# Performance work log

Hardware: AMD Instinct MI355X
Metric: run time of the kernel (lower is better)

The kernel has to match this reference:

```python
import jax, jax.numpy as jnp
import numpy as np

N = 20000   # genes
E = 200000  # global edges
P = 300     # pathways
EP = 2000   # edges per pathway (global node indices)
D = 3       # in_dim == number of omics (forced by nn.Linear(3,1))


def setup_inputs():
    key = jax.random.key(0)
    ks = jax.random.split(key, 20)
    f = lambda i, shape: jax.random.normal(ks[i], shape, dtype=jnp.float32) * 0.1
    return {
        "x": f(0, (N, D)),
        "edge_index": jax.random.randint(ks[1], (2, E), 0, N),
        "path_edges": jax.random.randint(ks[2], (P, 2, EP), 0, N),
        "W_pool": f(3, (D, D)), "b_pool": f(4, (D,)),
        "W_self": f(5, (D, D)), "W_neigh": f(6, (D, D)), "b_conv": f(7, (D,)),
        "sub_Wl": f(8, (P, D, D)), "sub_bl": f(9, (P, D)), "sub_Wr": f(10, (P, D, D)),
        "pool_Wrel": f(11, (P, D, 1)), "pool_Wroot": f(12, (P, D, 1)), "pool_b": f(13, (P, 1)),
        "gate_W": f(14, (P, D, 1)), "gate_b": f(15, (P, 1)),
        "lin_W": f(16, (D, 1)), "lin_b": f(17, (1,)),
        "mlp_W": f(18, (P, 1)), "mlp_b": f(19, (1,)),
    }


def reference(x, edge_index, path_edges, W_pool, b_pool, W_self, W_neigh, b_conv,
              sub_Wl, sub_bl, sub_Wr, pool_Wrel, pool_Wroot, pool_b,
              gate_W, gate_b, lin_W, lin_b, mlp_W, mlp_b):
    n = x.shape[0]
    # add_self_loops on the global edge_index
    loops = jnp.arange(n)
    src = jnp.concatenate([edge_index[0], loops])
    dst = jnp.concatenate([edge_index[1], loops])

    # global SAGEConv with 'pool' aggregator: max_j relu(W_pool h_j), then self + neigh
    hp = jax.nn.relu(x @ W_pool + b_pool)                       # [N,D]
    agg = jax.ops.segment_max(hp[src], dst, num_segments=n)     # [N,D] (self-loops -> no empty segments)
    h = jnp.tanh(x @ W_self + agg @ W_neigh + b_conv)           # [N,D]

    k = int(np.ceil(0.8 * n))  # SAGPooling ratio=0.8 over all N nodes (full x is passed per pathway)

    def per_path(pe, Wl, bl, Wr, Wrel, Wroot, pb, gW, gb):
        s, d = pe[0], pe[1]
        # SAGEConv (mean aggr) on pathway subgraph edges over full node set
        msum = jax.ops.segment_sum(h[s], d, num_segments=n)
        cnt = jax.ops.segment_sum(jnp.ones(s.shape, h.dtype), d, num_segments=n)
        mean = msum / jnp.maximum(cnt, 1.0)[:, None]
        xc = jax.nn.relu(mean @ Wl + bl + h @ Wr)               # [N,D]
        # SAGPooling score via GraphConv (add aggr): W_rel * sum_j x_j + W_root * x + b
        asum = jax.ops.segment_sum(xc[s], d, num_segments=n)
        score = (asum @ Wrel + xc @ Wroot + pb)[:, 0]           # [N]
        topv, perm = jax.lax.top_k(score, k)
        xk = xc[perm] * jnp.tanh(topv)[:, None]                 # [k,D]
        # GlobalAttention readout: softmax gate over kept nodes
        gate = jax.nn.softmax((xk @ gW + gb)[:, 0])             # [k]
        return jax.nn.relu(gate @ xk)                            # [D]

    readout = jax.vmap(per_path)(path_edges, sub_Wl, sub_bl, sub_Wr,
                                 pool_Wrel, pool_Wroot, pool_b, gate_W, gate_b)  # [P,D]
    r = jax.nn.relu(readout @ lin_W + lin_b).T                  # [1,P]
    # mlp: Dropout (identity in eval) -> ReLU -> Linear(P,1) -> Sigmoid
    return jax.nn.sigmoid(jax.nn.relu(r) @ mlp_W + mlp_b)       # [1,1]
```

## Files before the change

kernel.cpp:

```cpp
#include <hip/hip_runtime.h>
#include <math.h>

#define MAXM 2048
#define BMW  640
#define BS   1024
#define NB   2048

__device__ __forceinline__ unsigned fkey(float f){
  unsigned u = __float_as_uint(f);
  return (u & 0x80000000u) ? ~u : (u | 0x80000000u);
}
__device__ __forceinline__ int lbin(float sc, float lo, float scl){
  int b = (int)((sc - lo) * scl);
  return b < 0 ? 0 : (b > NB-1 ? NB-1 : b);
}
__device__ __forceinline__ float fast_tanh(float x){
  float e = __expf(2.f*x);
  return 1.f - 2.f*__builtin_amdgcn_rcpf(e + 1.f);
}
__device__ __forceinline__ void hp_eval(const float* __restrict__ x, int i,
                                        const float* __restrict__ Wp,
                                        const float* __restrict__ bp, float* o){
  float x0 = x[i*3+0], x1 = x[i*3+1], x2 = x[i*3+2];
  #pragma unroll
  for (int j = 0; j < 3; ++j)
    o[j] = fmaxf(x0*Wp[0*3+j] + x1*Wp[1*3+j] + x2*Wp[2*3+j] + bp[j], 0.f);
}

__global__ void k_edge(const float* __restrict__ x, const int* __restrict__ ei,
                       const float* __restrict__ Wp, const float* __restrict__ bp,
                       float* __restrict__ agg, float* __restrict__ acc,
                       unsigned* __restrict__ counter, int E){
  if (blockIdx.x == 0 && threadIdx.x == 0){ acc[0] = 0.f; counter[0] = 0u; }
  int e = blockIdx.x*blockDim.x + threadIdx.x;
  if (e >= E) return;
  int s = ei[e], d = ei[E+e];
  float o[3]; hp_eval(x, s, Wp, bp, o);
  #pragma unroll
  for (int j = 0; j < 3; ++j)
    if (o[j] > 0.f && o[j] > agg[d*4+j])
      atomicMax((int*)&agg[d*4+j], __float_as_int(o[j]));
}

__global__ void k_h2(const float* __restrict__ x, float* __restrict__ hb,
                     const float* __restrict__ Wp, const float* __restrict__ bp,
                     const float* __restrict__ Ws, const float* __restrict__ Wn,
                     const float* __restrict__ bc, int N){
  int i = blockIdx.x*blockDim.x + threadIdx.x;
  if (i >= N) return;
  float hp[3]; hp_eval(x, i, Wp, bp, hp);
  float x0 = x[i*3+0], x1 = x[i*3+1], x2 = x[i*3+2];
  float a0 = fmaxf(hb[i*4+0], hp[0]);
  float a1 = fmaxf(hb[i*4+1], hp[1]);
  float a2 = fmaxf(hb[i*4+2], hp[2]);
  float o[3];
  #pragma unroll
  for (int j = 0; j < 3; ++j){
    float v = x0*Ws[0*3+j] + x1*Ws[1*3+j] + x2*Ws[2*3+j]
            + a0*Wn[0*3+j] + a1*Wn[1*3+j] + a2*Wn[2*3+j] + bc[j];
    o[j] = tanhf(v);
  }
  float4 hv; hv.x = o[0]; hv.y = o[1]; hv.z = o[2]; hv.w = 0.f;
  *reinterpret_cast<float4*>(&hb[i*4]) = hv;
}

__global__ void __launch_bounds__(BS)
k_mega(const float* __restrict__ h, const int* __restrict__ pe,
       const float* __restrict__ sWl, const float* __restrict__ sbl, const float* __restrict__ sWr,
       const float* __restrict__ pWrel, const float* __restrict__ pWroot, const float* __restrict__ pB,
       const float* __restrict__ gW, const float* __restrict__ gB,
       const float* __restrict__ linW, const float* __restrict__ linb,
       const float* __restrict__ mlpW, const float* __restrict__ mlpb,
       float* __restrict__ spG, float* __restrict__ acc, unsigned* __restrict__ counter,
       unsigned* __restrict__ out, int N, int EP, int K, int P){
  __shared__ unsigned bm[BMW];
  __shared__ int      wpfx[BMW];
  __shared__ float    msum[MAXM*4];
  __shared__ unsigned scrA[NB];
  __shared__ unsigned scrB[NB];
  __shared__ unsigned candIdx[NB];
  __shared__ float    wredf[(BS/64)*2];
  __shared__ float    wredA[(BS/64)*4];
  __shared__ float    wredB[(BS/64)*4];
  __shared__ float    s_mn, s_mx;
  __shared__ float    s_slo, s_sscl;
  __shared__ float    rlo[3], rsc[3];
  __shared__ int      rb[3];
  __shared__ int      s_r, s_C, s_cc, s_done, s_fused;
  __shared__ unsigned s_uT;

  const int p = blockIdx.x;
  const int tid = threadIdx.x;

  float Wl[9], Wr[9], bl[3], wrel[3], wroot[3], gw[3];
  #pragma unroll
  for (int j = 0; j < 9; ++j){ Wl[j] = sWl[p*9+j]; Wr[j] = sWr[p*9+j]; }
  #pragma unroll
  for (int j = 0; j < 3; ++j){
    bl[j] = sbl[p*3+j]; wrel[j] = pWrel[p*3+j];
    wroot[j] = pWroot[p*3+j]; gw[j] = gW[p*3+j];
  }
  float pbv = pB[p], gbv = gB[p];
  float* sp = spG + (size_t)p*N;

  int*      cnt  = (int*)scrA;
  float*    adot = (float*)scrB;
  unsigned* hist = scrA;
  unsigned* cand = scrB;

  for (int s = tid; s < MAXM; s += BS){
    cnt[s] = 0; adot[s] = 0.f;
    float4 z; z.x = 0.f; z.y = 0.f; z.z = 0.f; z.w = 0.f;
    *reinterpret_cast<float4*>(&msum[s*4]) = z;
  }
  for (int s = tid; s < BMW; s += BS) bm[s] = 0u;
  if (tid == 0){ s_done = 0; s_fused = 0; s_uT = 0u; }
  __syncthreads();

  const int* ps = pe + (size_t)p*2*EP;
  const int* pd = ps + EP;

  for (int e = tid; e < EP; e += BS) atomicOr(&bm[pd[e]>>5], 1u << (pd[e]&31));
  __syncthreads();
  if (tid < 64){
    int l = tid, base = l*10;
    int c[10], s = 0;
    #pragma unroll
    for (int q = 0; q < 10; ++q){ c[q] = __popc(bm[base+q]); s += c[q]; }
    int pre = s;
    #pragma unroll
    for (int off = 1; off < 64; off <<= 1){
      int t = __shfl_up(pre, off);
      if (l >= off) pre += t;
    }
    pre -= s;
    #pragma unroll
    for (int q = 0; q < 10; ++q){ wpfx[base+q] = pre; pre += c[q]; }
  }
  __syncthreads();
  for (int e = tid; e < EP; e += BS){
    int s = ps[e], d = pd[e];
    int r = wpfx[d>>5] + __popc(bm[d>>5] & ((1u << (d&31)) - 1u));
    float4 hs = *reinterpret_cast<const float4*>(&h[s*4]);
    atomicAdd(&cnt[r], 1);
    atomicAdd(&msum[r*4+0], hs.x);
    atomicAdd(&msum[r*4+1], hs.y);
    atomicAdd(&msum[r*4+2], hs.z);
  }
  __syncthreads();
  for (int r = tid; r < MAXM; r += BS){
    int c = cnt[r];
    cnt[r] = 0;
    if (c > 0){
      float inv = 1.f / (float)c;
      msum[r*4+0] *= inv; msum[r*4+1] *= inv; msum[r*4+2] *= inv;
    }
  }
  __syncthreads();
  for (int e = tid; e < EP; e += BS){
    int s = ps[e], d = pd[e];
    float m0=0.f,m1=0.f,m2=0.f;
    unsigned w = bm[s>>5];
    if ((w >> (s&31)) & 1u){
      int rs = wpfx[s>>5] + __popc(w & ((1u << (s&31)) - 1u));
      float4 mv = *reinterpret_cast<const float4*>(&msum[rs*4]);
      m0 = mv.x; m1 = mv.y; m2 = mv.z;
    }
    float4 hv = *reinterpret_cast<const float4*>(&h[s*4]);
    float h0 = hv.x, h1 = hv.y, h2 = hv.z;
    float x0 = fmaxf(m0*Wl[0]+m1*Wl[3]+m2*Wl[6] + bl[0] + h0*Wr[0]+h1*Wr[3]+h2*Wr[6], 0.f);
    float x1 = fmaxf(m0*Wl[1]+m1*Wl[4]+m2*Wl[7] + bl[1] + h0*Wr[1]+h1*Wr[4]+h2*Wr[7], 0.f);
    float x2 = fmaxf(m0*Wl[2]+m1*Wl[5]+m2*Wl[8] + bl[2] + h0*Wr[2]+h1*Wr[5]+h2*Wr[8], 0.f);
    int rd = wpfx[d>>5] + __popc(bm[d>>5] & ((1u << (d&31)) - 1u));
    atomicAdd(&adot[rd], x0*wrel[0] + x1*wrel[1] + x2*wrel[2]);
  }
  __syncthreads();

  {
    int i = (int)(((long long)tid * (long long)N) / BS);
    float m0=0.f,m1=0.f,m2=0.f,ad=0.f;
    unsigned w = bm[i>>5];
    if ((w >> (i&31)) & 1u){
      int r = wpfx[i>>5] + __popc(w & ((1u << (i&31)) - 1u));
      float4 mv = *reinterpret_cast<const float4*>(&msum[r*4]);
      m0 = mv.x; m1 = mv.y; m2 = mv.z;
      ad = adot[r];
    }
    float4 hv = *reinterpret_cast<const float4*>(&h[i*4]);
    float h0 = hv.x, h1 = hv.y, h2 = hv.z;
    float x0 = fmaxf(m0*Wl[0]+m1*Wl[3]+m2*Wl[6] + bl[0] + h0*Wr[0]+h1*Wr[3]+h2*Wr[6], 0.f);
    float x1 = fmaxf(m0*Wl[1]+m1*Wl[4]+m2*Wl[7] + bl[1] + h0*Wr[1]+h1*Wr[4]+h2*Wr[7], 0.f);
    float x2 = fmaxf(m0*Wl[2]+m1*Wl[5]+m2*Wl[8] + bl[2] + h0*Wr[2]+h1*Wr[5]+h2*Wr[8], 0.f);
    float sc = ad + x0*wroot[0]+x1*wroot[1]+x2*wroot[2] + pbv;
    float smn = sc, smx = sc;
    #pragma unroll
    for (int off = 32; off > 0; off >>= 1){
      smn = fminf(smn, __shfl_down(smn, off));
      smx = fmaxf(smx, __shfl_down(smx, off));
    }
    if ((tid & 63) == 0){ int w2 = tid >> 6; wredf[w2*2+0] = smn; wredf[w2*2+1] = smx; }
    __syncthreads();
    if (tid == 0){
      float a = 3.0e38f, b = -3.0e38f;
      for (int w2 = 0; w2 < BS/64; ++w2){
        a = fminf(a, wredf[w2*2+0]); b = fmaxf(b, wredf[w2*2+1]);
      }
      float span = b - a;
      if (!(span > 0.f)) span = fabsf(a)*1e-6f + 1e-30f;
      s_slo = a; s_sscl = 2047.0f / span;
    }
    __syncthreads();
  }
  float lo0, scl0;
  {
    unsigned ulo = __builtin_amdgcn_readfirstlane(__float_as_uint(s_slo));
    unsigned usc = __builtin_amdgcn_readfirstlane(__float_as_uint(s_sscl));
    lo0 = __uint_as_float(ulo); scl0 = __uint_as_float(usc);
  }

  float mn = 3.0e38f, mx = -3.0e38f;
  float tl = 0.f, ta0 = 0.f, ta1 = 0.f, ta2 = 0.f;
  for (int i = tid; i < N; i += BS){
    float m0=0.f,m1=0.f,m2=0.f,ad=0.f;
    unsigned w = bm[i>>5];
    if ((w >> (i&31)) & 1u){
      int r = wpfx[i>>5] + __popc(w & ((1u << (i&31)) - 1u));
      float4 mv = *reinterpret_cast<const float4*>(&msum[r*4]);
      m0 = mv.x; m1 = mv.y; m2 = mv.z;
      ad = adot[r];
    }
    float4 hv = *reinterpret_cast<const float4*>(&h[i*4]);
    float h0 = hv.x, h1 = hv.y, h2 = hv.z;
    float x0 = fmaxf(m0*Wl[0]+m1*Wl[3]+m2*Wl[6] + bl[0] + h0*Wr[0]+h1*Wr[3]+h2*Wr[6], 0.f);
    float x1 = fmaxf(m0*Wl[1]+m1*Wl[4]+m2*Wl[7] + bl[1] + h0*Wr[1]+h1*Wr[4]+h2*Wr[7], 0.f);
    float x2 = fmaxf(m0*Wl[2]+m1*Wl[5]+m2*Wl[8] + bl[2] + h0*Wr[2]+h1*Wr[5]+h2*Wr[8], 0.f);
    float sc = ad + x0*wroot[0]+x1*wroot[1]+x2*wroot[2] + pbv;
    sp[i] = sc;
    atomicAdd(&hist[lbin(sc, lo0, scl0)], 1u);
    mn = fminf(mn, sc); mx = fmaxf(mx, sc);
    float tt = fast_tanh(sc);
    float g = fminf(fmaxf(tt*(x0*gw[0]+x1*gw[1]+x2*gw[2]) + gbv, -60.f), 60.f);
    float e = __expf(g);
    float et = e * tt;
    tl += e; ta0 += et*x0; ta1 += et*x1; ta2 += et*x2;
  }
  #pragma unroll
  for (int off = 32; off > 0; off >>= 1){
    mn  = fminf(mn, __shfl_down(mn, off));
    mx  = fmaxf(mx, __shfl_down(mx, off));
    tl  += __shfl_down(tl,  off); ta0 += __shfl_down(ta0, off);
    ta1 += __shfl_down(ta1, off); ta2 += __shfl_down(ta2, off);
  }
  if ((tid & 63) == 0){
    int w = tid >> 6;
    wredf[w*2+0] = mn; wredf[w*2+1] = mx;
    wredA[w*4+0]=tl; wredA[w*4+1]=ta0; wredA[w*4+2]=ta1; wredA[w*4+3]=ta2;
  }
  __syncthreads();
  if (tid == 0){
    float a = 3.0e38f, b = -3.0e38f;
    for (int w = 0; w < BS/64; ++w){ a = fminf(a, wredf[w*2+0]); b = fmaxf(b, wredf[w*2+1]); }
    s_mn = a; s_mx = b; s_r = K;
    if (!(b > a)){ s_uT = fkey(a); s_done = 1; s_fused = 1; }
  }
  __syncthreads();

  float dl = 0.f, d0 = 0.f, d1 = 0.f, d2 = 0.f;

  for (int t = 0; t < 3; ++t){
    __syncthreads();
    if (s_done) break;
    float lo, scl;
    if (t == 0){
      lo = s_slo; scl = s_sscl;
    } else {
      float plo = rlo[t-1], pscl = rsc[t-1]; int pb = rb[t-1];
      lo = plo + pb/pscl;
      float hi = plo + (pb+1)/pscl;
      if (t == 1){
        if (pb == 0)    lo = s_mn;
        if (pb == NB-1) hi = s_mx;
      }
      scl = 2047.0f / (hi - lo);
      if (!(hi > lo) || !(scl < 1e37f)){
        if (tid == 0){ s_uT = fkey(lo); s_done = 1; }
        __syncthreads();
        continue;
      }
      for (int b = tid; b < NB; b += BS) hist[b] = 0u;
      __syncthreads();
      for (int i = tid; i < N; i += BS){
        float sc = sp[i];
        bool act = true;
        for (int q = 0; q < t; ++q) act = act && (lbin(sc, rlo[q], rsc[q]) == rb[q]);
        if (act) atomicAdd(&hist[lbin(sc, lo, scl)], 1u);
      }
      __syncthreads();
    }
    if (tid < 64){
      int l = tid;
      unsigned s = 0;
      for (int q = 0; q < 32; ++q) s += hist[l*32+q];
      unsigned S = s;
      #pragma unroll
      for (int off = 1; off < 64; off <<= 1){
        unsigned u2 = __shfl_down(S, off);
        if (l + off < 64) S += u2;
      }
      unsigned suf = S - s;
      unsigned r = (unsigned)s_r;
      int b = -1; unsigned sufnext = 0, cb = 0;
      for (int q = 31; q >= 0; --q){
        unsigned c = hist[l*32+q];
        unsigned nsuf = suf + c;
        if (nsuf >= r && suf < r){ b = l*32+q; sufnext = suf; cb = c; }
        suf = nsuf;
      }
      if (b >= 0){
        rb[t] = b; rlo[t] = lo; rsc[t] = scl;
        s_r = (int)(r - sufnext);
        s_C = (int)cb;
      }
    }
    __syncthreads();
    int C = s_C;
    if (C <= NB){
      if (tid < 1024) hist[tid] = 0u;
      if (tid == 0) s_cc = 0;
      __syncthreads();
      if (t == 0 && (N & 3) == 0){
        const int b0 = rb[0];
        const float l0 = rlo[0], s0 = rsc[0];
        int G = N >> 2;
        for (int g = tid; g < G; g += BS){
          float4 v = ((const float4*)sp)[g];
          #pragma unroll
          for (int u = 0; u < 4; ++u){
            float sc = (u==0)?v.x:((u==1)?v.y:((u==2)?v.z:v.w));
            int b = lbin(sc, l0, s0);
            if (b == b0){
              int ix = atomicAdd(&s_cc, 1);
              if (ix < NB){ cand[ix] = fkey(sc); candIdx[ix] = (unsigned)(g*4+u); }
            } else if (b < b0){
              int i = g*4+u;
              float m0=0.f,m1=0.f,m2=0.f;
              unsigned w = bm[i>>5];
              if ((w >> (i&31)) & 1u){
                int r = wpfx[i>>5] + __popc(w & ((1u << (i&31)) - 1u));
                float4 mv = *reinterpret_cast<const float4*>(&msum[r*4]);
                m0 = mv.x; m1 = mv.y; m2 = mv.z;
              }
              float4 hv = *reinterpret_cast<const float4*>(&h[i*4]);
              float h0 = hv.x, h1 = hv.y, h2 = hv.z;
              float x0 = fmaxf(m0*Wl[0]+m1*Wl[3]+m2*Wl[6] + bl[0] + h0*Wr[0]+h1*Wr[3]+h2*Wr[6], 0.f);
              float x1 = fmaxf(m0*Wl[1]+m1*Wl[4]+m2*Wl[7] + bl[1] + h0*Wr[1]+h1*Wr[4]+h2*Wr[7], 0.f);
              float x2 = fmaxf(m0*Wl[2]+m1*Wl[5]+m2*Wl[8] + bl[2] + h0*Wr[2]+h1*Wr[5]+h2*Wr[8], 0.f);
              float tt = fast_tanh(sc);
              float gg = fminf(fmaxf(tt*(x0*gw[0]+x1*gw[1]+x2*gw[2]) + gbv, -60.f), 60.f);
              float e = __expf(gg);
              float et = e * tt;
              dl += e; d0 += et*x0; d1 += et*x1; d2 += et*x2;
            }
          }
        }
      } else {
        for (int i = tid; i < N; i += BS){
          float sc = sp[i];
          bool iscand = true, isdrop = false;
          for (int q = 0; q <= t; ++q){
            int b = lbin(sc, rlo[q], rsc[q]);
            if (b != rb[q]){ iscand = false; isdrop = (b < rb[q]); break; }
          }
          if (iscand){
            int ix = atomicAdd(&s_cc, 1);
            if (ix < NB){ cand[ix] = fkey(sc); candIdx[ix] = (unsigned)i; }
          } else if (isdrop){
            float m0=0.f,m1=0.f,m2=0.f;
            unsigned w = bm[i>>5];
            if ((w >> (i&31)) & 1u){
              int r = wpfx[i>>5] + __popc(w & ((1u << (i&31)) - 1u));
              float4 mv = *reinterpret_cast<const float4*>(&msum[r*4]);
              m0 = mv.x; m1 = mv.y; m2 = mv.z;
            }
            float4 hv = *reinterpret_cast<const float4*>(&h[i*4]);
            float h0 = hv.x, h1 = hv.y, h2 = hv.z;
            float x0 = fmaxf(m0*Wl[0]+m1*Wl[3]+m2*Wl[6] + bl[0] + h0*Wr[0]+h1*Wr[3]+h2*Wr[6], 0.f);
            float x1 = fmaxf(m0*Wl[1]+m1*Wl[4]+m2*Wl[7] + bl[1] + h0*Wr[1]+h1*Wr[4]+h2*Wr[7], 0.f);
            float x2 = fmaxf(m0*Wl[2]+m1*Wl[5]+m2*Wl[8] + bl[2] + h0*Wr[2]+h1*Wr[5]+h2*Wr[8], 0.f);
            float tt = fast_tanh(sc);
            float gg = fminf(fmaxf(tt*(x0*gw[0]+x1*gw[1]+x2*gw[2]) + gbv, -60.f), 60.f);
            float e = __expf(gg);
            float et = e * tt;
            dl += e; d0 += et*x0; d1 += et*x1; d2 += et*x2;
          }
        }
      }
      __syncthreads();
      if (tid < 64){
        int l = tid;
        unsigned pref = 0u, mask = 0u;
        int r = s_r;
        #pragma unroll
        for (int pass = 0; pass < 4; ++pass){
          int shift = 24 - 8*pass;
          unsigned* hp = hist + (pass << 8);
          for (int j = l; j < C; j += 64){
            unsigned u = cand[j];
            if ((u & mask) == pref) atomicAdd(&hp[(u>>shift)&255u], 1u);
          }
          asm volatile("s_waitcnt lgkmcnt(0)" ::: "memory");
          unsigned h0 = hp[4*l+0], h1 = hp[4*l+1], h2 = hp[4*l+2], h3 = hp[4*l+3];
          unsigned ssum = h0+h1+h2+h3;
          unsigned S = ssum;
          #pragma unroll
          for (int off = 1; off < 64; off <<= 1){
            unsigned u2 = __shfl_down(S, off);
            if (l + off < 64) S += u2;
          }
          unsigned Snext = S - ssum;
          unsigned rr = (unsigned)r;
          unsigned suf3 = h3 + Snext;
          unsigned suf2 = h2 + suf3;
          unsigned suf1 = h1 + suf2;
          unsigned suf0 = h0 + suf1;
          int b = -1; unsigned sufn = 0;
          if      (suf3 >= rr && Snext < rr){ b = 4*l+3; sufn = Snext; }
          else if (suf2 >= rr && suf3  < rr){ b = 4*l+2; sufn = suf3; }
          else if (suf1 >= rr && suf2  < rr){ b = 4*l+1; sufn = suf2; }
          else if (suf0 >= rr && suf1  < rr){ b = 4*l+0; sufn = suf1; }
          unsigned long long ball = __ballot(b >= 0);
          int src = __ffsll(ball) - 1;
          b    = __shfl(b, src);
          sufn = (unsigned)__shfl((int)sufn, src);
          pref |= (unsigned)b << shift;
          mask |= 255u << shift;
          r = (int)(rr - sufn);
        }
        if (l == 0) s_uT = pref;
      }
      if (tid == 0){ s_done = 1; s_fused = 1; }
      __syncthreads();
      {
        const unsigned uTl = s_uT;
        for (int j = tid; j < C; j += BS){
          if (cand[j] < uTl){
            int i = (int)candIdx[j];
            float sc = sp[i];
            float m0=0.f,m1=0.f,m2=0.f;
            unsigned w = bm[i>>5];
            if ((w >> (i&31)) & 1u){
              int r = wpfx[i>>5] + __popc(w & ((1u << (i&31)) - 1u));
              float4 mv = *reinterpret_cast<const float4*>(&msum[r*4]);
              m0 = mv.x; m1 = mv.y; m2 = mv.z;
            }
            float4 hv = *reinterpret_cast<const float4*>(&h[i*4]);
            float h0 = hv.x, h1 = hv.y, h2 = hv.z;
            float x0 = fmaxf(m0*Wl[0]+m1*Wl[3]+m2*Wl[6] + bl[0] + h0*Wr[0]+h1*Wr[3]+h2*Wr[6], 0.f);
            float x1 = fmaxf(m0*Wl[1]+m1*Wl[4]+m2*Wl[7] + bl[1] + h0*Wr[1]+h1*Wr[4]+h2*Wr[7], 0.f);
            float x2 = fmaxf(m0*Wl[2]+m1*Wl[5]+m2*Wl[8] + bl[2] + h0*Wr[2]+h1*Wr[5]+h2*Wr[8], 0.f);
            float tt = fast_tanh(sc);
            float gg = fminf(fmaxf(tt*(x0*gw[0]+x1*gw[1]+x2*gw[2]) + gbv, -60.f), 60.f);
            float e = __expf(gg);
            float et = e * tt;
            dl += e; d0 += et*x0; d1 += et*x1; d2 += et*x2;
          }
        }
      }
    } else if (t == 2){
      if (tid == 0){ s_uT = fkey(lo + rb[t]/scl); s_done = 1; }
      __syncthreads();
    }
  }
  __syncthreads();
  const unsigned uT = s_uT;

  if (!s_fused){
    for (int i = tid; i < N; i += BS){
      float sc = sp[i];
      if (fkey(sc) < uT){
        float m0=0.f,m1=0.f,m2=0.f;
        unsigned w = bm[i>>5];
        if ((w >> (i&31)) & 1u){
          int r = wpfx[i>>5] + __popc(w & ((1u << (i&31)) - 1u));
          float4 mv = *reinterpret_cast<const float4*>(&msum[r*4]);
          m0 = mv.x; m1 = mv.y; m2 = mv.z;
        }
        float4 hv = *reinterpret_cast<const float4*>(&h[i*4]);
        float h0 = hv.x, h1 = hv.y, h2 = hv.z;
        float x0 = fmaxf(m0*Wl[0]+m1*Wl[3]+m2*Wl[6] + bl[0] + h0*Wr[0]+h1*Wr[3]+h2*Wr[6], 0.f);
        float x1 = fmaxf(m0*Wl[1]+m1*Wl[4]+m2*Wl[7] + bl[1] + h0*Wr[1]+h1*Wr[4]+h2*Wr[7], 0.f);
        float x2 = fmaxf(m0*Wl[2]+m1*Wl[5]+m2*Wl[8] + bl[2] + h0*Wr[2]+h1*Wr[5]+h2*Wr[8], 0.f);
        float tt = fast_tanh(sc);
        float gg = fminf(fmaxf(tt*(x0*gw[0]+x1*gw[1]+x2*gw[2]) + gbv, -60.f), 60.f);
        float e = __expf(gg);
        float et = e * tt;
        dl += e; d0 += et*x0; d1 += et*x1; d2 += et*x2;
      }
    }
  }
  #pragma unroll
  for (int off = 32; off > 0; off >>= 1){
    dl += __shfl_down(dl, off); d0 += __shfl_down(d0, off);
    d1 += __shfl_down(d1, off); d2 += __shfl_down(d2, off);
  }
  if ((tid & 63) == 0){
    int w = tid >> 6;
    wredB[w*4+0]=dl; wredB[w*4+1]=d0; wredB[w*4+2]=d1; wredB[w*4+3]=d2;
  }
  __syncthreads();
  if (tid == 0){
    float L=0.f, A0=0.f, A1=0.f, A2=0.f;
    for (int w = 0; w < BS/64; ++w){
      L  += wredA[w*4+0] - wredB[w*4+0];
      A0 += wredA[w*4+1] - wredB[w*4+1];
      A1 += wredA[w*4+2] - wredB[w*4+2];
      A2 += wredA[w*4+3] - wredB[w*4+3];
    }
    float inv = 1.f / L;
    float r0 = fmaxf(A0*inv, 0.f);
    float r1 = fmaxf(A1*inv, 0.f);
    float r2 = fmaxf(A2*inv, 0.f);
    float rr = fmaxf(r0*linW[0] + r1*linW[1] + r2*linW[2] + linb[0], 0.f);
    atomicAdd(acc, rr * mlpW[p]);
    __threadfence();
    unsigned old = atomicAdd(counter, 1u);
    if (old == (unsigned)(P-1)){
      __threadfence();
      float z = atomicAdd(acc, 0.f) + mlpb[0];
      float a = 1.f / (1.f + expf(-z));
      unsigned A = __float_as_uint(a);
      unsigned B = (A + 0x7FFFu + ((A >> 16) & 1u)) >> 16;
      out[0] = (A & 0xFFFF0000u) | (B & 0xFFFFu);
    }
  }
}

extern "C" void kernel_launch(void* const* d_in, const int* in_sizes, int n_in,
                              void* d_out, int out_size, void* d_ws, size_t ws_size,
                              hipStream_t stream){
  const float* x      = (const float*)d_in[0];
  const int*   ei     = (const int*)  d_in[1];
  const int*   pe     = (const int*)  d_in[2];
  const float* W_pool = (const float*)d_in[3];
  const float* b_pool = (const float*)d_in[4];
  const float* W_self = (const float*)d_in[5];
  const float* W_neigh= (const float*)d_in[6];
  const float* b_conv = (const float*)d_in[7];
  const float* sWl    = (const float*)d_in[8];
  const float* sbl    = (const float*)d_in[9];
  const float* sWr    = (const float*)d_in[10];
  const float* pWrel  = (const float*)d_in[11];
  const float* pWroot = (const float*)d_in[12];
  const float* pB     = (const float*)d_in[13];
  const float* gW     = (const float*)d_in[14];
  const float* gB     = (const float*)d_in[15];
  const float* linW   = (const float*)d_in[16];
  const float* linb   = (const float*)d_in[17];
  const float* mlpW   = (const float*)d_in[18];
  const float* mlpb   = (const float*)d_in[19];

  const int N  = in_sizes[0] / 3;
  const int E  = in_sizes[1] / 2;
  const int P  = in_sizes[13];
  const int EP = in_sizes[2] / (2 * P);
  const int K  = (4*N + 4) / 5;

  float*    ws      = (float*)d_ws;
  float*    acc     = ws;
  unsigned* counter = (unsigned*)(ws + 1);
  float*    agg     = ws + 16;
  float*    h       = agg;
  float*    spG     = ws + 16 + (size_t)4*N;

  k_edge<<<(E+255)/256, 256, 0, stream>>>(x, ei, W_pool, b_pool, agg, acc, counter, E);
  k_h2  <<<(N+255)/256, 256, 0, stream>>>(x, agg, W_pool, b_pool,
                                          W_self, W_neigh, b_conv, N);
  k_mega<<<P, BS, 0, stream>>>(h, pe, sWl, sbl, sWr, pWrel, pWroot, pB, gW, gB,
                               linW, linb, mlpW, mlpb,
                               spG, acc, counter, (unsigned*)d_out, N, EP, K, P);
}
```

Baseline: 229.7 us.

## Predict top-k threshold window from sample and capture candidates in main pass

Builds a histogram from a 1024-sample of scores to estimate the top-k boundary bin, then during the main scoring pass directly accumulates dropped-node contributions below the window and captures candidates inside a ±WIN bin window into shared memory. If the real boundary bin falls inside the window and capacity holds, the second full rescan of the score array is skipped and the radix select runs on the captured candidates. This adds an extra 8KB shared array, a sample-histogram reduction step, and per-element branching/atomics in the main loop, with a fallback path when the prediction misses.

Result: slower. 240.3 us (+4.6%).

```diff
diff --git a/kernel.cpp b/kernel.cpp
--- a/kernel.cpp
+++ b/kernel.cpp
@@ -5,6 +5,7 @@
 #define BMW  640
 #define BS   1024
 #define NB   2048
+#define WIN  40
 
 __device__ __forceinline__ unsigned fkey(float f){
   unsigned u = __float_as_uint(f);
@@ -79,6 +80,7 @@
   __shared__ unsigned scrA[NB];
   __shared__ unsigned scrB[NB];
   __shared__ unsigned candIdx[NB];
+  __shared__ unsigned capK[NB];
   __shared__ float    wredf[(BS/64)*2];
   __shared__ float    wredA[(BS/64)*4];
   __shared__ float    wredB[(BS/64)*4];
@@ -87,6 +89,7 @@
   __shared__ float    rlo[3], rsc[3];
   __shared__ int      rb[3];
   __shared__ int      s_r, s_C, s_cc, s_done, s_fused;
+  __shared__ int      s_wlo, s_whi, s_fastok;
   __shared__ unsigned s_uT;
 
   const int p = blockIdx.x;
@@ -109,12 +112,12 @@
   unsigned* cand = scrB;
 
   for (int s = tid; s < MAXM; s += BS){
-    cnt[s] = 0; adot[s] = 0.f;
+    cnt[s] = 0; adot[s] = 0.f; candIdx[s] = 0u;
     float4 z; z.x = 0.f; z.y = 0.f; z.z = 0.f; z.w = 0.f;
     *reinterpret_cast<float4*>(&msum[s*4]) = z;
   }
   for (int s = tid; s < BMW; s += BS) bm[s] = 0u;
-  if (tid == 0){ s_done = 0; s_fused = 0; s_uT = 0u; }
+  if (tid == 0){ s_done = 0; s_fused = 0; s_uT = 0u; s_cc = 0; s_fastok = 0; }
   __syncthreads();
 
   const int* ps = pe + (size_t)p*2*EP;
@@ -176,6 +179,7 @@
   }
   __syncthreads();
 
+  float lo0, scl0;
   {
     int i = (int)(((long long)tid * (long long)N) / BS);
     float m0=0.f,m1=0.f,m2=0.f,ad=0.f;
@@ -210,13 +214,44 @@
       s_slo = a; s_sscl = 2047.0f / span;
     }
     __syncthreads();
-  }
-  float lo0, scl0;
-  {
-    unsigned ulo = __builtin_amdgcn_readfirstlane(__float_as_uint(s_slo));
-    unsigned usc = __builtin_amdgcn_readfirstlane(__float_as_uint(s_sscl));
-    lo0 = __uint_as_float(ulo); scl0 = __uint_as_float(usc);
-  }
+    {
+      unsigned ulo = __builtin_amdgcn_readfirstlane(__float_as_uint(s_slo));
+      unsigned usc = __builtin_amdgcn_readfirstlane(__float_as_uint(s_sscl));
+      lo0 = __uint_as_float(ulo); scl0 = __uint_as_float(usc);
+    }
+    atomicAdd(&candIdx[lbin(sc, lo0, scl0)], 1u);
+    __syncthreads();
+    if (tid < 64){
+      int rs = (int)(((long long)K * BS) / N);
+      if (rs < 1) rs = 1; if (rs > BS) rs = BS;
+      int l = tid;
+      unsigned s = 0;
+      for (int q = 0; q < 32; ++q) s += candIdx[l*32+q];
+      unsigned S = s;
+      #pragma unroll
+      for (int off = 1; off < 64; off <<= 1){
+        unsigned u2 = __shfl_down(S, off);
+        if (l + off < 64) S += u2;
+      }
+      unsigned suf = S - s;
+      int b = -1;
+      for (int q = 31; q >= 0; --q){
+        unsigned c = candIdx[l*32+q];
+        unsigned nsuf = suf + c;
+        if (nsuf >= (unsigned)rs && suf < (unsigned)rs) b = l*32+q;
+        suf = nsuf;
+      }
+      if (b >= 0){
+        s_wlo = (b - WIN < 0) ? 0 : b - WIN;
+        s_whi = (b + WIN > NB-1) ? NB-1 : b + WIN;
+      }
+    }
+    __syncthreads();
+  }
+  const int wloR = __builtin_amdgcn_readfirstlane(s_wlo);
+  const int whiR = __builtin_amdgcn_readfirstlane(s_whi);
+
+  float dl = 0.f, d0 = 0.f, d1 = 0.f, d2 = 0.f;
 
   float mn = 3.0e38f, mx = -3.0e38f;
   float tl = 0.f, ta0 = 0.f, ta1 = 0.f, ta2 = 0.f;
@@ -236,13 +271,20 @@
     float x2 = fmaxf(m0*Wl[2]+m1*Wl[5]+m2*Wl[8] + bl[2] + h0*Wr[2]+h1*Wr[5]+h2*Wr[8], 0.f);
     float sc = ad + x0*wroot[0]+x1*wroot[1]+x2*wroot[2] + pbv;
     sp[i] = sc;
-    atomicAdd(&hist[lbin(sc, lo0, scl0)], 1u);
+    int bin = lbin(sc, lo0, scl0);
+    atomicAdd(&hist[bin], 1u);
     mn = fminf(mn, sc); mx = fmaxf(mx, sc);
     float tt = fast_tanh(sc);
     float g = fminf(fmaxf(tt*(x0*gw[0]+x1*gw[1]+x2*gw[2]) + gbv, -60.f), 60.f);
     float e = __expf(g);
     float et = e * tt;
     tl += e; ta0 += et*x0; ta1 += et*x1; ta2 += et*x2;
+    if (bin < wloR){
+      dl += e; d0 += et*x0; d1 += et*x1; d2 += et*x2;
+    } else if (bin <= whiR){
+      int ix = atomicAdd(&s_cc, 1);
+      if (ix < NB){ capK[ix] = fkey(sc); candIdx[ix] = (unsigned)i; }
+    }
   }
   #pragma unroll
   for (int off = 32; off > 0; off >>= 1){
@@ -264,8 +306,6 @@
     if (!(b > a)){ s_uT = fkey(a); s_done = 1; s_fused = 1; }
   }
   __syncthreads();
-
-  float dl = 0.f, d0 = 0.f, d1 = 0.f, d2 = 0.f;
 
   for (int t = 0; t < 3; ++t){
     __syncthreads();
@@ -323,26 +363,75 @@
       }
     }
     __syncthreads();
+    if (t == 0){
+      if (tid < 64){
+        int b0v = rb[0];
+        int ok = (s_cc <= NB) && (s_C <= NB) && (b0v >= s_wlo) && (b0v <= s_whi);
+        unsigned abv = 0u;
+        if (ok){
+          for (int q = b0v + 1 + tid; q <= s_whi; q += 64) abv += hist[q];
+          #pragma unroll
+          for (int off = 32; off > 0; off >>= 1) abv += __shfl_down(abv, off);
+        }
+        if (tid == 0){ s_fastok = ok ? 1 : 0; if (ok) s_r += (int)abv; }
+      }
+      __syncthreads();
+      if (!s_fastok){ dl = 0.f; d0 = 0.f; d1 = 0.f; d2 = 0.f; }
+    }
     int C = s_C;
     if (C <= NB){
+      const bool fast = (t == 0) && (s_fastok != 0);
       if (tid < 1024) hist[tid] = 0u;
-      if (tid == 0) s_cc = 0;
+      if (!fast && tid == 0) s_cc = 0;
       __syncthreads();
-      if (t == 0 && (N & 3) == 0){
-        const int b0 = rb[0];
-        const float l0 = rlo[0], s0 = rsc[0];
-        int G = N >> 2;
-        for (int g = tid; g < G; g += BS){
-          float4 v = ((const float4*)sp)[g];
-          #pragma unroll
-          for (int u = 0; u < 4; ++u){
-            float sc = (u==0)?v.x:((u==1)?v.y:((u==2)?v.z:v.w));
-            int b = lbin(sc, l0, s0);
-            if (b == b0){
+      if (!fast){
+        if (t == 0 && (N & 3) == 0){
+          const int b0 = rb[0];
+          const float l0 = rlo[0], s0 = rsc[0];
+          int G = N >> 2;
+          for (int g = tid; g < G; g += BS){
+            float4 v = ((const float4*)sp)[g];
+            #pragma unroll
+            for (int u = 0; u < 4; ++u){
+              float sc = (u==0)?v.x:((u==1)?v.y:((u==2)?v.z:v.w));
+              int b = lbin(sc, l0, s0);
+              if (b == b0){
+                int ix = atomicAdd(&s_cc, 1);
+                if (ix < NB){ cand[ix] = fkey(sc); candIdx[ix] = (unsigned)(g*4+u); }
+              } else if (b < b0){
+                int i = g*4+u;
+                float m0=0.f,m1=0.f,m2=0.f;
+                unsigned w = bm[i>>5];
+                if ((w >> (i&31)) & 1u){
+                  int r = wpfx[i>>5] + __popc(w & ((1u << (i&31)) - 1u));
+                  float4 mv = *reinterpret_cast<const float4*>(&msum[r*4]);
+                  m0 = mv.x; m1 = mv.y; m2 = mv.z;
+                }
+                float4 hv = *reinterpret_cast<const float4*>(&h[i*4]);
+                float h0 = hv.x, h1 = hv.y, h2 = hv.z;
+                float x0 = fmaxf(m0*Wl[0]+m1*Wl[3]+m2*Wl[6] + bl[0] + h0*Wr[0]+h1*Wr[3]+h2*Wr[6], 0.f);
+                float x1 = fmaxf(m0*Wl[1]+m1*Wl[4]+m2*Wl[7] + bl[1] + h0*Wr[1]+h1*Wr[4]+h2*Wr[7], 0.f);
+                float x2 = fmaxf(m0*Wl[2]+m1*Wl[5]+m2*Wl[8] + bl[2] + h0*Wr[2]+h1*Wr[5]+h2*Wr[8], 0.f);
+                float tt = fast_tanh(sc);
+                float gg = fminf(fmaxf(tt*(x0*gw[0]+x1*gw[1]+x2*gw[2]) + gbv, -60.f), 60.f);
+                float e = __expf(gg);
+                float et = e * tt;
+                dl += e; d0 += et*x0; d1 += et*x1; d2 += et*x2;
+              }
+            }
+          }
+        } else {
+          for (int i = tid; i < N; i += BS){
+            float sc = sp[i];
+            bool iscand = true, isdrop = false;
+            for (int q = 0; q <= t; ++q){
+              int b = lbin(sc, rlo[q], rsc[q]);
+              if (b != rb[q]){ iscand = false; isdrop = (b < rb[q]); break; }
+            }
+            if (iscand){
               int ix = atomicAdd(&s_cc, 1);
-              if (ix < NB){ cand[ix] = fkey(sc); candIdx[ix] = (unsigned)(g*4+u); }
-            } else if (b < b0){
-              int i = g*4+u;
+              if (ix < NB){ cand[ix] = fkey(sc); candIdx[ix] = (unsigned)i; }
+            } else if (isdrop){
               float m0=0.f,m1=0.f,m2=0.f;
               unsigned w = bm[i>>5];
               if ((w >> (i&31)) & 1u){
@@ -363,39 +452,10 @@
             }
           }
         }
-      } else {
-        for (int i = tid; i < N; i += BS){
-          float sc = sp[i];
-          bool iscand = true, isdrop = false;
-          for (int q = 0; q <= t; ++q){
-            int b = lbin(sc, rlo[q], rsc[q]);
-            if (b != rb[q]){ iscand = false; isdrop = (b < rb[q]); break; }
-          }
-          if (iscand){
-            int ix = atomicAdd(&s_cc, 1);
-            if (ix < NB){ cand[ix] = fkey(sc); candIdx[ix] = (unsigned)i; }
-          } else if (isdrop){
-            float m0=0.f,m1=0.f,m2=0.f;
-            unsigned w = bm[i>>5];
-            if ((w >> (i&31)) & 1u){
-              int r = wpfx[i>>5] + __popc(w & ((1u << (i&31)) - 1u));
-              float4 mv = *reinterpret_cast<const float4*>(&msum[r*4]);
-              m0 = mv.x; m1 = mv.y; m2 = mv.z;
-            }
-            float4 hv = *reinterpret_cast<const float4*>(&h[i*4]);
-            float h0 = hv.x, h1 = hv.y, h2 = hv.z;
-            float x0 = fmaxf(m0*Wl[0]+m1*Wl[3]+m2*Wl[6] + bl[0] + h0*Wr[0]+h1*Wr[3]+h2*Wr[6], 0.f);
-            float x1 = fmaxf(m0*Wl[1]+m1*Wl[4]+m2*Wl[7] + bl[1] + h0*Wr[1]+h1*Wr[4]+h2*Wr[7], 0.f);
-            float x2 = fmaxf(m0*Wl[2]+m1*Wl[5]+m2*Wl[8] + bl[2] + h0*Wr[2]+h1*Wr[5]+h2*Wr[8], 0.f);
-            float tt = fast_tanh(sc);
-            float gg = fminf(fmaxf(tt*(x0*gw[0]+x1*gw[1]+x2*gw[2]) + gbv, -60.f), 60.f);
-            float e = __expf(gg);
-            float et = e * tt;
-            dl += e; d0 += et*x0; d1 += et*x1; d2 += et*x2;
-          }
-        }
       }
       __syncthreads();
+      unsigned* CND = fast ? capK : cand;
+      int CC = fast ? (s_cc < NB ? s_cc : NB) : C;
       if (tid < 64){
         int l = tid;
         unsigned pref = 0u, mask = 0u;
@@ -404,8 +464,8 @@
         for (int pass = 0; pass < 4; ++pass){
           int shift = 24 - 8*pass;
           unsigned* hp = hist + (pass << 8);
-          for (int j = l; j < C; j += 64){
-            unsigned u = cand[j];
+          for (int j = l; j < CC; j += 64){
+            unsigned u = CND[j];
             if ((u & mask) == pref) atomicAdd(&hp[(u>>shift)&255u], 1u);
           }
           asm volatile("s_waitcnt lgkmcnt(0)" ::: "memory");
@@ -442,8 +502,8 @@
       __syncthreads();
       {
         const unsigned uTl = s_uT;
-        for (int j = tid; j < C; j += BS){
-          if (cand[j] < uTl){
+        for (int j = tid; j < CC; j += BS){
+          if (CND[j] < uTl){
             int i = (int)candIdx[j];
             float sc = sp[i];
             float m0=0.f,m1=0.f,m2=0.f;
```
